# Performance work log

Measured on AMD Instinct MI355X. Metric: run time of the kernel, lower is better.

Reference implementation:

```python
import jax, jax.numpy as jnp
import numpy as np

N = 100000      # nodes
E = 600000      # directed edges (before self-loops)
NFEAT = 128
NHID = 128
NCLASS = 64


def setup_inputs() -> dict:
    key = jax.random.key(0)
    k1, k2, k3, k4 = jax.random.split(key, 4)
    x = jax.random.normal(k1, (N, NFEAT), dtype=jnp.float32)
    edge_index = jax.random.randint(k2, (2, E), 0, N, dtype=jnp.int32)
    # GCNConv learned params (Glorot-ish init), bias zeros as in PyG default
    W1 = jax.random.normal(k3, (NFEAT, NHID), dtype=jnp.float32) / jnp.sqrt(NFEAT)
    b1 = jnp.zeros((NHID,), dtype=jnp.float32)
    W2 = jax.random.normal(k4, (NHID, NCLASS), dtype=jnp.float32) / jnp.sqrt(NHID)
    b2 = jnp.zeros((NCLASS,), dtype=jnp.float32)
    return {"x": x, "edge_index": edge_index, "W1": W1, "b1": b1, "W2": W2, "b2": b2}


def _gcn_layer(x, src, dst, norm, W, b, n):
    # PyG GCNConv: linear transform, then normalized neighbor aggregation, then bias
    h = x @ W                                   # [N, out]
    msg = h[src] * norm[:, None]                # [E+N, out] gather + scale
    agg = jax.ops.segment_sum(msg, dst, num_segments=n)  # scatter-add
    return agg + b


def reference(x, edge_index, W1, b1, W2, b2):
    n = x.shape[0]
    # add self-loops (PyG gcn_norm default add_self_loops=True)
    loops = jnp.arange(n, dtype=edge_index.dtype)
    src = jnp.concatenate([edge_index[0], loops])
    dst = jnp.concatenate([edge_index[1], loops])
    # symmetric normalization: D^-1/2 (A+I) D^-1/2
    deg = jax.ops.segment_sum(jnp.ones_like(dst, dtype=x.dtype), dst, num_segments=n)
    d_inv_sqrt = jnp.where(deg > 0, jax.lax.rsqrt(deg), 0.0)
    norm = d_inv_sqrt[src] * d_inv_sqrt[dst]
    h = jax.nn.relu(_gcn_layer(x, src, dst, norm, W1, b1, n))
    # F.dropout with training=False is identity -> omitted in eval reference
    return _gcn_layer(h, src, dst, norm, W2, b2, n)
```

## Files before the change

### kernel.cpp

```cpp
#include <hip/hip_runtime.h>


typedef unsigned short u16;
typedef unsigned int u32;
typedef __attribute__((ext_vector_type(8))) short bf16x8;
typedef __attribute__((ext_vector_type(4))) float f32x4;

__device__ __forceinline__ float b2f(u16 s) {
  return __uint_as_float(((u32)s) << 16);
}
__device__ __forceinline__ u16 f2b(float f) {
  u32 u = __float_as_uint(f);
  u32 r = (u + 0x7FFFu + ((u >> 16) & 1u)) >> 16;
  return (u16)r;
}
__device__ __forceinline__ u32 pk2(float a, float b) {
  return (u32)f2b(a) | ((u32)f2b(b) << 16);
}
__device__ __forceinline__ void dec8(uint4 v, float f[8]) {
  f[0] = __uint_as_float(v.x << 16);
  f[1] = __uint_as_float(v.x & 0xFFFF0000u);
  f[2] = __uint_as_float(v.y << 16);
  f[3] = __uint_as_float(v.y & 0xFFFF0000u);
  f[4] = __uint_as_float(v.z << 16);
  f[5] = __uint_as_float(v.z & 0xFFFF0000u);
  f[6] = __uint_as_float(v.w << 16);
  f[7] = __uint_as_float(v.w & 0xFFFF0000u);
}
__device__ __forceinline__ void fma8(uint4 v, float d, float acc[8]) {
  acc[0] = fmaf(__uint_as_float(v.x << 16), d, acc[0]);
  acc[1] = fmaf(__uint_as_float(v.x & 0xFFFF0000u), d, acc[1]);
  acc[2] = fmaf(__uint_as_float(v.y << 16), d, acc[2]);
  acc[3] = fmaf(__uint_as_float(v.y & 0xFFFF0000u), d, acc[3]);
  acc[4] = fmaf(__uint_as_float(v.z << 16), d, acc[4]);
  acc[5] = fmaf(__uint_as_float(v.z & 0xFFFF0000u), d, acc[5]);
  acc[6] = fmaf(__uint_as_float(v.w << 16), d, acc[6]);
  acc[7] = fmaf(__uint_as_float(v.w & 0xFFFF0000u), d, acc[7]);
}


__global__ __launch_bounds__(256) void prep_k(const void* __restrict__ W1,
                                              const void* __restrict__ b1,
                                              const void* __restrict__ W2,
                                              const void* __restrict__ b2,
                                              u16* __restrict__ W1b, u16* __restrict__ ob1,
                                              u16* __restrict__ W2t, u16* __restrict__ ob2,
                                              int* __restrict__ mode,
                                              int* __restrict__ cnt, int np) {
  __shared__ int cnt_s;
  const int tid = threadIdx.x;
  int i = blockIdx.x * 256 + tid;
  if (i < np) cnt[i] = 0;

  if (tid == 0) cnt_s = 0;
  __syncthreads();
  int c = 0;
  for (int j = tid; j < 4096; j += 256) {
    u32 e = (((const u16*)W1)[j] >> 7) & 0xFFu;
    if (e >= 100u && e <= 130u) c++;
  }
  atomicAdd(&cnt_s, c);
  __syncthreads();
  const int m = (cnt_s < 3328) ? 1 : 0;
  if (blockIdx.x == 0 && tid == 0) *mode = m;

  if (i < 24768) {
    int j = i;
    const void* src;
    u16* dst;
    int sidx, didx;
    if (j < 16384) {
      src = W1; dst = W1b; sidx = j; didx = j;
    } else if ((j -= 16384) < 128) {
      src = b1; dst = ob1; sidx = j; didx = j;
    } else if ((j -= 128) < 8192) {
      int nn = j >> 7, k = j & 127;
      src = W2; dst = W2t; sidx = k * 64 + nn; didx = j;
    } else {
      j -= 8192;
      src = b2; dst = ob2; sidx = j; didx = j;
    }
    dst[didx] = m ? f2b(((const float*)src)[sidx]) : ((const u16*)src)[sidx];
  }
}


__global__ __launch_bounds__(256) void count_k(const int* __restrict__ dst,
                                               int* __restrict__ cnt, int E) {
  int e = blockIdx.x * 256 + threadIdx.x;
  if (e < E) atomicAdd(&cnt[dst[e]], 1);
}

__global__ __launch_bounds__(256) void scan1(const int* __restrict__ cnt,
                                             int* __restrict__ offs,
                                             int* __restrict__ bsum, int np) {
  __shared__ int lds[256];
  int t = threadIdx.x;
  int i = blockIdx.x * 256 + t;
  int v = cnt[i];
  lds[t] = v;
  __syncthreads();
#pragma unroll
  for (int off = 1; off < 256; off <<= 1) {
    int add = (t >= off) ? lds[t - off] : 0;
    __syncthreads();
    lds[t] += add;
    __syncthreads();
  }
  offs[i] = lds[t] - v;
  if (t == 0) bsum[blockIdx.x] = lds[255];
}

__global__ __launch_bounds__(256) void scan23(const int* __restrict__ offs,
                                              const int* __restrict__ bsum,
                                              int* __restrict__ cursor,
                                              const int* __restrict__ cnt,
                                              float* __restrict__ dinv,
                                              int4* __restrict__ ninfo, int np) {
  __shared__ int lds[256];
  const int t = threadIdx.x, b = blockIdx.x;
  int part = 0;
  for (int k = t; k < b; k += 256) part += bsum[k];
  lds[t] = part;
  __syncthreads();
#pragma unroll
  for (int off = 128; off > 0; off >>= 1) {
    if (t < off) lds[t] += lds[t + off];
    __syncthreads();
  }
  const int pre = lds[0];
  int i = b * 256 + t;
  int o = offs[i] + pre;
  cursor[i] = o;
  int c = cnt[i];
  float dv = rsqrtf((float)c + 1.0f);
  dinv[i] = dv;
  ninfo[i] = make_int4(o, c, __float_as_int(dv), 0);
}

__global__ __launch_bounds__(256) void fill_k(const int* __restrict__ src,
                                              const int* __restrict__ dst,
                                              int* __restrict__ cursor,
                                              const float* __restrict__ dinv,
                                              int2* __restrict__ sp, int E) {
  int e = blockIdx.x * 256 + threadIdx.x;
  if (e < E) {
    int s = src[e];
    float ds = dinv[s];
    int p = atomicAdd(&cursor[dst[e]], 1);
    sp[p] = make_int2(s, __float_as_int(ds));
  }
}


__global__ __launch_bounds__(256) void gemm1_k(const void* __restrict__ Araw,
                                               const u16* __restrict__ W,
                                               u16* __restrict__ out, int M,
                                               const int* __restrict__ mode) {
  __shared__ __align__(16) u16 Wt[128 * 136];
  __shared__ __align__(16) u16 As[64 * 136];
  const int tid = threadIdx.x;
  const int mcv = *mode;

  for (int idx = tid; idx < 128 * 128; idx += 256) {
    int n = idx & 127;
    int k = idx >> 7;
    Wt[n * 136 + k] = W[k * 128 + n];
  }
  __syncthreads();

  const int wv = tid >> 6, lane = tid & 63, lr = lane & 15, lq = lane >> 4;
  const int ntiles = (M + 63) >> 6;

  for (int t = blockIdx.x; t < ntiles; t += gridDim.x) {
    const int r0 = t * 64;
    __syncthreads();
    for (int idx = tid; idx < 64 * 16; idx += 256) {
      int row = idx >> 4, c = idx & 15;
      uint4 v = make_uint4(0u, 0u, 0u, 0u);
      if (r0 + row < M) {
        if (mcv) {
          const float* xf = (const float*)Araw + (size_t)(r0 + row) * 128 + c * 8;
          float4 f0 = *(const float4*)xf;
          float4 f1 = *(const float4*)(xf + 4);
          v.x = pk2(f0.x, f0.y);
          v.y = pk2(f0.z, f0.w);
          v.z = pk2(f1.x, f1.y);
          v.w = pk2(f1.z, f1.w);
        } else {
          v = *(const uint4*)((const u16*)Araw + (size_t)(r0 + row) * 128 + c * 8);
        }
      }
      *(uint4*)&As[row * 136 + c * 8] = v;
    }
    __syncthreads();

    bf16x8 a[4];
#pragma unroll
    for (int s = 0; s < 4; ++s)
      a[s] = *(const bf16x8*)&As[(wv * 16 + lr) * 136 + s * 32 + lq * 8];

#pragma unroll
    for (int nt = 0; nt < 8; ++nt) {
      f32x4 acc = {0.f, 0.f, 0.f, 0.f};
#pragma unroll
      for (int s = 0; s < 4; ++s) {
        bf16x8 b = *(const bf16x8*)&Wt[(nt * 16 + lr) * 136 + s * 32 + lq * 8];
        acc = __builtin_amdgcn_mfma_f32_16x16x32_bf16(a[s], b, acc, 0, 0, 0);
      }
#pragma unroll
      for (int r = 0; r < 4; ++r) {
        int row = r0 + wv * 16 + lq * 4 + r;
        if (row < M) out[(size_t)row * 128 + nt * 16 + lr] = f2b(acc[r]);
      }
    }
  }
}


__global__ __launch_bounds__(256) void fusedB_k(const u16* __restrict__ h,
                                                const int2* __restrict__ sp,
                                                const int4* __restrict__ ninfo,
                                                const u16* __restrict__ b1,
                                                const u16* __restrict__ W2t,
                                                u16* __restrict__ g, int n) {
  __shared__ __align__(16) u16 As[16 * 136];
  const int tid = threadIdx.x, wv = tid >> 6, lane = tid & 63;
  const int lq = lane >> 4, lr = lane & 15;
  const int base = blockIdx.x * 16;
  const int i = base + wv * 4 + lq;
  const bool valid = (i < n);

  int start = 0, c = 0;
  float di = 0.f;
  if (valid) {
    int4 ni = ninfo[i];
    start = ni.x;
    c = ni.y;
    di = __int_as_float(ni.z);
  }
  float acc[8];
  {
    uint4 v = valid ? *(const uint4*)(h + (size_t)i * 128 + lr * 8)
                    : make_uint4(0u, 0u, 0u, 0u);
    float f[8];
    dec8(v, f);
#pragma unroll
    for (int j = 0; j < 8; ++j) acc[j] = f[j] * di;
  }
  const int bl = lq * 16;
  for (int bs = 0; __any(bs < c); bs += 16) {
    int m = c - bs;
    m = m < 0 ? 0 : (m > 16 ? 16 : m);
    int s = 0, db = 0;
    if (lr < m) {
      int2 p = sp[start + bs + lr];
      s = p.x;
      db = p.y;
    }
    int mmw = m;
    mmw = max(mmw, __shfl_xor(mmw, 16));
    mmw = max(mmw, __shfl_xor(mmw, 32));
    for (int e = 0; e < mmw; e += 4) {
      int s0 = __shfl(s, bl + e), s1 = __shfl(s, bl + e + 1);
      int s2 = __shfl(s, bl + e + 2), s3 = __shfl(s, bl + e + 3);
      float d0 = __int_as_float(__shfl(db, bl + e));
      float d1 = __int_as_float(__shfl(db, bl + e + 1));
      float d2 = __int_as_float(__shfl(db, bl + e + 2));
      float d3 = __int_as_float(__shfl(db, bl + e + 3));
      uint4 v0 = *(const uint4*)(h + (size_t)s0 * 128 + lr * 8);
      uint4 v1 = *(const uint4*)(h + (size_t)s1 * 128 + lr * 8);
      uint4 v2 = *(const uint4*)(h + (size_t)s2 * 128 + lr * 8);
      uint4 v3 = *(const uint4*)(h + (size_t)s3 * 128 + lr * 8);
      fma8(v0, d0, acc);
      fma8(v1, d1, acc);
      fma8(v2, d2, acc);
      fma8(v3, d3, acc);
    }
  }
  {
    uint4 bv = *(const uint4*)(b1 + lr * 8);
    float bf[8];
    dec8(bv, bf);
    float o[8];
#pragma unroll
    for (int j = 0; j < 8; ++j) o[j] = fmaxf(fmaf(acc[j], di, bf[j]), 0.f);
    uint4 ov;
    ov.x = pk2(o[0], o[1]);
    ov.y = pk2(o[2], o[3]);
    ov.z = pk2(o[4], o[5]);
    ov.w = pk2(o[6], o[7]);
    *(uint4*)&As[(wv * 4 + lq) * 136 + lr * 8] = ov;
  }
  __syncthreads();

  bf16x8 a[4];
#pragma unroll
  for (int s = 0; s < 4; ++s)
    a[s] = *(const bf16x8*)&As[lr * 136 + s * 32 + lq * 8];
  {
    const int nt = wv;
    f32x4 acc4 = {0.f, 0.f, 0.f, 0.f};
#pragma unroll
    for (int s = 0; s < 4; ++s) {
      bf16x8 b = *(const bf16x8*)&W2t[(nt * 16 + lr) * 128 + s * 32 + lq * 8];
      acc4 = __builtin_amdgcn_mfma_f32_16x16x32_bf16(a[s], b, acc4, 0, 0, 0);
    }
#pragma unroll
    for (int r = 0; r < 4; ++r) {
      int row = base + lq * 4 + r;
      if (row < n) g[(size_t)row * 64 + nt * 16 + lr] = f2b(acc4[r]);
    }
  }
}


__global__ __launch_bounds__(256) void agg2_k(const u16* __restrict__ g,
                                              const int2* __restrict__ sp,
                                              const int4* __restrict__ ninfo,
                                              const u16* __restrict__ b2,
                                              void* __restrict__ outv, int n,
                                              const int* __restrict__ mode) {
  const int lane = threadIdx.x & 63;
  const int o8 = lane >> 3, l8 = lane & 7;
  const int i = blockIdx.x * 32 + (threadIdx.x >> 6) * 8 + o8;
  const bool valid = (i < n);

  int start = 0, c = 0;
  float di = 0.f;
  if (valid) {
    int4 ni = ninfo[i];
    start = ni.x;
    c = ni.y;
    di = __int_as_float(ni.z);
  }
  float acc[8];
  {
    uint4 v = valid ? *(const uint4*)(g + (size_t)i * 64 + l8 * 8)
                    : make_uint4(0u, 0u, 0u, 0u);
    float f[8];
    dec8(v, f);
#pragma unroll
    for (int j = 0; j < 8; ++j) acc[j] = f[j] * di;
  }
  const int bl = o8 * 8;
  for (int base = 0; __any(base < c); base += 8) {
    int m = c - base;
    m = m < 0 ? 0 : (m > 8 ? 8 : m);
    int s = 0, db = 0;
    if (l8 < m) {
      int2 p = sp[start + base + l8];
      s = p.x;
      db = p.y;
    }
    int mmw = m;
    mmw = max(mmw, __shfl_xor(mmw, 8));
    mmw = max(mmw, __shfl_xor(mmw, 16));
    mmw = max(mmw, __shfl_xor(mmw, 32));
    for (int e = 0; e < mmw; e += 4) {
      int s0 = __shfl(s, bl + e), s1 = __shfl(s, bl + e + 1);
      int s2 = __shfl(s, bl + e + 2), s3 = __shfl(s, bl + e + 3);
      float d0 = __int_as_float(__shfl(db, bl + e));
      float d1 = __int_as_float(__shfl(db, bl + e + 1));
      float d2 = __int_as_float(__shfl(db, bl + e + 2));
      float d3 = __int_as_float(__shfl(db, bl + e + 3));
      uint4 v0 = *(const uint4*)(g + (size_t)s0 * 64 + l8 * 8);
      uint4 v1 = *(const uint4*)(g + (size_t)s1 * 64 + l8 * 8);
      uint4 v2 = *(const uint4*)(g + (size_t)s2 * 64 + l8 * 8);
      uint4 v3 = *(const uint4*)(g + (size_t)s3 * 64 + l8 * 8);
      fma8(v0, d0, acc);
      fma8(v1, d1, acc);
      fma8(v2, d2, acc);
      fma8(v3, d3, acc);
    }
  }
  if (valid) {
    uint4 bv = *(const uint4*)(b2 + l8 * 8);
    float bf[8];
    dec8(bv, bf);
    float o[8];
#pragma unroll
    for (int j = 0; j < 8; ++j) o[j] = fmaf(acc[j], di, bf[j]);
    if (*mode) {
      float* op = (float*)outv + (size_t)i * 64 + l8 * 8;
      *(float4*)op = make_float4(o[0], o[1], o[2], o[3]);
      *(float4*)(op + 4) = make_float4(o[4], o[5], o[6], o[7]);
    } else {
      uint4 ov;
      ov.x = pk2(o[0], o[1]);
      ov.y = pk2(o[2], o[3]);
      ov.z = pk2(o[4], o[5]);
      ov.w = pk2(o[6], o[7]);
      *(uint4*)((u16*)outv + (size_t)i * 64 + l8 * 8) = ov;
    }
  }
}


extern "C" void kernel_launch(void* const* d_in, const int* in_sizes, int n_in,
                              void* d_out, int out_size, void* d_ws, size_t ws_size,
                              hipStream_t stream) {
  const void* x_raw  = d_in[0];
  const int*  ei     = (const int*)d_in[1];
  const void* W1_raw = d_in[2];
  const void* b1_raw = d_in[3];
  const void* W2_raw = d_in[4];
  const void* b2_raw = d_in[5];

  const int N = in_sizes[0] / 128;
  const int E = in_sizes[1] / 2;
  const int NP = ((N + 255) / 256) * 256;
  const int NB = NP / 256;

  char* ws = (char*)d_ws;
  size_t off = 0;
  auto alloc = [&](size_t bytes) -> void* {
    void* p = ws + off;
    off = (off + bytes + 255) & ~(size_t)255;
    return p;
  };
  int*   mode   = (int*)alloc(4);
  int*   cnt    = (int*)alloc((size_t)NP * 4);
  float* dinv   = (float*)alloc((size_t)NP * 4);
  int*   offs   = (int*)alloc((size_t)NP * 4);
  int*   cursor = (int*)alloc((size_t)NP * 4);
  int*   bsum   = (int*)alloc(1024 * 4);
  int4*  ninfo  = (int4*)alloc((size_t)NP * 16);
  int2*  sp     = (int2*)alloc((size_t)E * 8);
  u16*   W1b    = (u16*)alloc((size_t)128 * 128 * 2);
  u16*   b1b    = (u16*)alloc(128 * 2);
  u16*   W2t    = (u16*)alloc((size_t)64 * 128 * 2);
  u16*   b2b    = (u16*)alloc(64 * 2);
  u16*   h      = (u16*)alloc((size_t)N * 128 * 2);
  u16*   g      = (u16*)alloc((size_t)N * 64 * 2);

  const int eb = (E + 255) / 256;
  prep_k<<<NB, 256, 0, stream>>>(W1_raw, b1_raw, W2_raw, b2_raw,
                                 W1b, b1b, W2t, b2b, mode, cnt, NP);
  count_k<<<eb, 256, 0, stream>>>(ei + E, cnt, E);
  scan1<<<NB, 256, 0, stream>>>(cnt, offs, bsum, NP);
  scan23<<<NB, 256, 0, stream>>>(offs, bsum, cursor, cnt, dinv, ninfo, NP);
  fill_k<<<eb, 256, 0, stream>>>(ei, ei + E, cursor, dinv, sp, E);
  gemm1_k<<<512, 256, 0, stream>>>(x_raw, W1b, h, N, mode);
  fusedB_k<<<(N + 15) / 16, 256, 0, stream>>>(h, sp, ninfo, b1b, W2t, g, N);
  agg2_k<<<(N + 31) / 32, 256, 0, stream>>>(g, sp, ninfo, b2b, d_out, N, mode);
}
```

Measured before the change: 239.9 us.

## Prescale features by source dinv and store only source indices in CSR

Measured after the change: 243.5 us. About the same (+1.5%).

```diff
diff --git a/kernel.cpp b/kernel.cpp
--- a/kernel.cpp
+++ b/kernel.cpp
@@ -141,20 +141,24 @@
 __global__ __launch_bounds__(256) void fill_k(const int* __restrict__ src,
                                               const int* __restrict__ dst,
                                               int* __restrict__ cursor,
-                                              const float* __restrict__ dinv,
-                                              int2* __restrict__ sp, int E) {
-  int e = blockIdx.x * 256 + threadIdx.x;
-  if (e < E) {
-    int s = src[e];
-    float ds = dinv[s];
-    int p = atomicAdd(&cursor[dst[e]], 1);
-    sp[p] = make_int2(s, __float_as_int(ds));
-  }
+                                              int* __restrict__ sp, int E) {
+  int e0 = blockIdx.x * 512 + threadIdx.x;
+  int e1 = e0 + 256;
+  int s0 = 0, s1 = 0, d0 = 0, d1 = 0;
+  bool v0 = e0 < E, v1 = e1 < E;
+  if (v0) { s0 = src[e0]; d0 = dst[e0]; }
+  if (v1) { s1 = src[e1]; d1 = dst[e1]; }
+  int p0 = 0, p1 = 0;
+  if (v0) p0 = atomicAdd(&cursor[d0], 1);
+  if (v1) p1 = atomicAdd(&cursor[d1], 1);
+  if (v0) sp[p0] = s0;
+  if (v1) sp[p1] = s1;
 }
 
 
 __global__ __launch_bounds__(256) void gemm1_k(const void* __restrict__ Araw,
                                                const u16* __restrict__ W,
+                                               const float* __restrict__ dinv,
                                                u16* __restrict__ out, int M,
                                                const int* __restrict__ mode) {
   __shared__ __align__(16) u16 Wt[128 * 136];
@@ -200,6 +204,13 @@
     for (int s = 0; s < 4; ++s)
       a[s] = *(const bf16x8*)&As[(wv * 16 + lr) * 136 + s * 32 + lq * 8];
 
+    float dv[4];
+#pragma unroll
+    for (int r = 0; r < 4; ++r) {
+      int row = r0 + wv * 16 + lq * 4 + r;
+      dv[r] = (row < M) ? dinv[row] : 0.f;
+    }
+
 #pragma unroll
     for (int nt = 0; nt < 8; ++nt) {
       f32x4 acc = {0.f, 0.f, 0.f, 0.f};
@@ -211,19 +222,19 @@
 #pragma unroll
       for (int r = 0; r < 4; ++r) {
         int row = r0 + wv * 16 + lq * 4 + r;
-        if (row < M) out[(size_t)row * 128 + nt * 16 + lr] = f2b(acc[r]);
+        if (row < M) out[(size_t)row * 128 + nt * 16 + lr] = f2b(acc[r] * dv[r]);
       }
     }
   }
 }
 
 
-__global__ __launch_bounds__(256) void fusedB_k(const u16* __restrict__ h,
-                                                const int2* __restrict__ sp,
+__global__ __launch_bounds__(256) void fusedB_k(const u16* __restrict__ hs,
+                                                const int* __restrict__ sp,
                                                 const int4* __restrict__ ninfo,
                                                 const u16* __restrict__ b1,
                                                 const u16* __restrict__ W2t,
-                                                u16* __restrict__ g, int n) {
+                                                u16* __restrict__ gs, int n) {
   __shared__ __align__(16) u16 As[16 * 136];
   const int tid = threadIdx.x, wv = tid >> 6, lane = tid & 63;
   const int lq = lane >> 4, lr = lane & 15;
@@ -241,41 +252,34 @@
   }
   float acc[8];
   {
-    uint4 v = valid ? *(const uint4*)(h + (size_t)i * 128 + lr * 8)
+    uint4 v = valid ? *(const uint4*)(hs + (size_t)i * 128 + lr * 8)
                     : make_uint4(0u, 0u, 0u, 0u);
-    float f[8];
-    dec8(v, f);
-#pragma unroll
-    for (int j = 0; j < 8; ++j) acc[j] = f[j] * di;
+    dec8(v, acc);
   }
   const int bl = lq * 16;
   for (int bs = 0; __any(bs < c); bs += 16) {
     int m = c - bs;
     m = m < 0 ? 0 : (m > 16 ? 16 : m);
-    int s = 0, db = 0;
-    if (lr < m) {
-      int2 p = sp[start + bs + lr];
-      s = p.x;
-      db = p.y;
-    }
+    int s = 0;
+    if (lr < m) s = sp[start + bs + lr];
     int mmw = m;
     mmw = max(mmw, __shfl_xor(mmw, 16));
     mmw = max(mmw, __shfl_xor(mmw, 32));
     for (int e = 0; e < mmw; e += 4) {
       int s0 = __shfl(s, bl + e), s1 = __shfl(s, bl + e + 1);
       int s2 = __shfl(s, bl + e + 2), s3 = __shfl(s, bl + e + 3);
-      float d0 = __int_as_float(__shfl(db, bl + e));
-      float d1 = __int_as_float(__shfl(db, bl + e + 1));
-      float d2 = __int_as_float(__shfl(db, bl + e + 2));
-      float d3 = __int_as_float(__shfl(db, bl + e + 3));
-      uint4 v0 = *(const uint4*)(h + (size_t)s0 * 128 + lr * 8);
-      uint4 v1 = *(const uint4*)(h + (size_t)s1 * 128 + lr * 8);
-      uint4 v2 = *(const uint4*)(h + (size_t)s2 * 128 + lr * 8);
-      uint4 v3 = *(const uint4*)(h + (size_t)s3 * 128 + lr * 8);
-      fma8(v0, d0, acc);
-      fma8(v1, d1, acc);
-      fma8(v2, d2, acc);
-      fma8(v3, d3, acc);
+      float w0 = (e < m) ? 1.f : 0.f;
+      float w1 = (e + 1 < m) ? 1.f : 0.f;
+      float w2 = (e + 2 < m) ? 1.f : 0.f;
+      float w3 = (e + 3 < m) ? 1.f : 0.f;
+      uint4 v0 = *(const uint4*)(hs + (size_t)s0 * 128 + lr * 8);
+      uint4 v1 = *(const uint4*)(hs + (size_t)s1 * 128 + lr * 8);
+      uint4 v2 = *(const uint4*)(hs + (size_t)s2 * 128 + lr * 8);
+      uint4 v3 = *(const uint4*)(hs + (size_t)s3 * 128 + lr * 8);
+      fma8(v0, w0, acc);
+      fma8(v1, w1, acc);
+      fma8(v2, w2, acc);
+      fma8(v3, w3, acc);
     }
   }
   {
@@ -309,14 +313,17 @@
 #pragma unroll
     for (int r = 0; r < 4; ++r) {
       int row = base + lq * 4 + r;
-      if (row < n) g[(size_t)row * 64 + nt * 16 + lr] = f2b(acc4[r]);
-    }
-  }
-}
-
-
-__global__ __launch_bounds__(256) void agg2_k(const u16* __restrict__ g,
-                                              const int2* __restrict__ sp,
+      if (row < n) {
+        float dv = __int_as_float(((const int4*)ninfo)[row].z);
+        gs[(size_t)row * 64 + nt * 16 + lr] = f2b(acc4[r] * dv);
+      }
+    }
+  }
+}
+
+
+__global__ __launch_bounds__(256) void agg2_k(const u16* __restrict__ gs,
+                                              const int* __restrict__ sp,
                                               const int4* __restrict__ ninfo,
                                               const u16* __restrict__ b2,
                                               void* __restrict__ outv, int n,
@@ -336,23 +343,16 @@
   }
   float acc[8];
   {
-    uint4 v = valid ? *(const uint4*)(g + (size_t)i * 64 + l8 * 8)
+    uint4 v = valid ? *(const uint4*)(gs + (size_t)i * 64 + l8 * 8)
                     : make_uint4(0u, 0u, 0u, 0u);
-    float f[8];
-    dec8(v, f);
-#pragma unroll
-    for (int j = 0; j < 8; ++j) acc[j] = f[j] * di;
+    dec8(v, acc);
   }
   const int bl = o8 * 8;
   for (int base = 0; __any(base < c); base += 8) {
     int m = c - base;
     m = m < 0 ? 0 : (m > 8 ? 8 : m);
-    int s = 0, db = 0;
-    if (l8 < m) {
-      int2 p = sp[start + base + l8];
-      s = p.x;
-      db = p.y;
-    }
+    int s = 0;
+    if (l8 < m) s = sp[start + base + l8];
     int mmw = m;
     mmw = max(mmw, __shfl_xor(mmw, 8));
     mmw = max(mmw, __shfl_xor(mmw, 16));
@@ -360,18 +360,18 @@
     for (int e = 0; e < mmw; e += 4) {
       int s0 = __shfl(s, bl + e), s1 = __shfl(s, bl + e + 1);
       int s2 = __shfl(s, bl + e + 2), s3 = __shfl(s, bl + e + 3);
-      float d0 = __int_as_float(__shfl(db, bl + e));
-      float d1 = __int_as_float(__shfl(db, bl + e + 1));
-      float d2 = __int_as_float(__shfl(db, bl + e + 2));
-      float d3 = __int_as_float(__shfl(db, bl + e + 3));
-      uint4 v0 = *(const uint4*)(g + (size_t)s0 * 64 + l8 * 8);
-      uint4 v1 = *(const uint4*)(g + (size_t)s1 * 64 + l8 * 8);
-      uint4 v2 = *(const uint4*)(g + (size_t)s2 * 64 + l8 * 8);
-      uint4 v3 = *(const uint4*)(g + (size_t)s3 * 64 + l8 * 8);
-      fma8(v0, d0, acc);
-      fma8(v1, d1, acc);
-      fma8(v2, d2, acc);
-      fma8(v3, d3, acc);
+      float w0 = (e < m) ? 1.f : 0.f;
+      float w1 = (e + 1 < m) ? 1.f : 0.f;
+      float w2 = (e + 2 < m) ? 1.f : 0.f;
+      float w3 = (e + 3 < m) ? 1.f : 0.f;
+      uint4 v0 = *(const uint4*)(gs + (size_t)s0 * 64 + l8 * 8);
+      uint4 v1 = *(const uint4*)(gs + (size_t)s1 * 64 + l8 * 8);
+      uint4 v2 = *(const uint4*)(gs + (size_t)s2 * 64 + l8 * 8);
+      uint4 v3 = *(const uint4*)(gs + (size_t)s3 * 64 + l8 * 8);
+      fma8(v0, w0, acc);
+      fma8(v1, w1, acc);
+      fma8(v2, w2, acc);
+      fma8(v3, w3, acc);
     }
   }
   if (valid) {
@@ -426,13 +426,13 @@
   int*   cursor = (int*)alloc((size_t)NP * 4);
   int*   bsum   = (int*)alloc(1024 * 4);
   int4*  ninfo  = (int4*)alloc((size_t)NP * 16);
-  int2*  sp     = (int2*)alloc((size_t)E * 8);
+  int*   sp     = (int*)alloc((size_t)E * 4);
   u16*   W1b    = (u16*)alloc((size_t)128 * 128 * 2);
   u16*   b1b    = (u16*)alloc(128 * 2);
   u16*   W2t    = (u16*)alloc((size_t)64 * 128 * 2);
   u16*   b2b    = (u16*)alloc(64 * 2);
-  u16*   h      = (u16*)alloc((size_t)N * 128 * 2);
-  u16*   g      = (u16*)alloc((size_t)N * 64 * 2);
+  u16*   hs     = (u16*)alloc((size_t)N * 128 * 2);
+  u16*   gs     = (u16*)alloc((size_t)N * 64 * 2);
 
   const int eb = (E + 255) / 256;
   prep_k<<<NB, 256, 0, stream>>>(W1_raw, b1_raw, W2_raw, b2_raw,
@@ -440,8 +440,8 @@
   count_k<<<eb, 256, 0, stream>>>(ei + E, cnt, E);
   scan1<<<NB, 256, 0, stream>>>(cnt, offs, bsum, NP);
   scan23<<<NB, 256, 0, stream>>>(offs, bsum, cursor, cnt, dinv, ninfo, NP);
-  fill_k<<<eb, 256, 0, stream>>>(ei, ei + E, cursor, dinv, sp, E);
-  gemm1_k<<<512, 256, 0, stream>>>(x_raw, W1b, h, N, mode);
-  fusedB_k<<<(N + 15) / 16, 256, 0, stream>>>(h, sp, ninfo, b1b, W2t, g, N);
-  agg2_k<<<(N + 31) / 32, 256, 0, stream>>>(g, sp, ninfo, b2b, d_out, N, mode);
-}
+  fill_k<<<(E + 511) / 512, 256, 0, stream>>>(ei, ei + E, cursor, sp, E);
+  gemm1_k<<<512, 256, 0, stream>>>(x_raw, W1b, dinv, hs, N, mode);
+  fusedB_k<<<(N + 15) / 16, 256, 0, stream>>>(hs, sp, ninfo, b1b, W2t, gs, N);
+  agg2_k<<<(N + 31) / 32, 256, 0, stream>>>(gs, sp, ninfo, b2b, d_out, N, mode);
+}
```
